# Optimization experiments

Measured on AMD Instinct MI355X. Metric: run time of the kernel, lower is better.

## Reference

```python
import jax, jax.numpy as jnp
import numpy as np

H = 768
F = 3072
NH = 12
EPS = 1e-5


def _layer_norm(x, g, b):
    mu = jnp.mean(x, axis=-1, keepdims=True)
    var = jnp.mean(jnp.square(x - mu), axis=-1, keepdims=True)
    return (x - mu) * jax.lax.rsqrt(var + EPS) * g + b


def setup_inputs() -> dict:
    key = jax.random.key(0)
    ks = jax.random.split(key, 16)
    s = 0.02
    d = {
        'x': jax.random.normal(ks[0], (2, 2048, H), jnp.float32),
        'Wq': jax.random.normal(ks[1], (H, H), jnp.float32) * s,
        'bq': jnp.zeros((H,), jnp.float32),
        'Wk': jax.random.normal(ks[2], (H, H), jnp.float32) * s,
        'bk': jnp.zeros((H,), jnp.float32),
        'Wv': jax.random.normal(ks[3], (H, H), jnp.float32) * s,
        'bv': jnp.zeros((H,), jnp.float32),
        'Wa1': jax.random.normal(ks[4], (H, H), jnp.float32) * s,
        'ba1': jnp.zeros((H,), jnp.float32),
        'g1': jnp.ones((H,), jnp.float32),
        'be1': jnp.zeros((H,), jnp.float32),
        'W1': jax.random.normal(ks[5], (H, F), jnp.float32) * s,
        'b1': jnp.zeros((F,), jnp.float32),
        'W2': jax.random.normal(ks[6], (F, H), jnp.float32) * s,
        'b2': jnp.zeros((H,), jnp.float32),
        'Wa2': jax.random.normal(ks[7], (H, H), jnp.float32) * s,
        'ba2': jnp.zeros((H,), jnp.float32),
        'g2': jnp.ones((H,), jnp.float32),
        'be2': jnp.zeros((H,), jnp.float32),
    }
    return d


def reference(x, Wq, bq, Wk, bk, Wv, bv, Wa1, ba1, g1, be1, W1, b1, W2, b2, Wa2, ba2, g2, be2):
    B, S, _ = x.shape
    Dh = H // NH
    # multi-head attention (naive: explicit scores + softmax)
    q = (x @ Wq + bq).reshape(B, S, NH, Dh)
    k = (x @ Wk + bk).reshape(B, S, NH, Dh)
    v = (x @ Wv + bv).reshape(B, S, NH, Dh)
    scores = jnp.einsum('bqhd,bkhd->bhqk', q, k) / jnp.sqrt(jnp.float32(Dh))
    att = jax.nn.softmax(scores, axis=-1)
    ctx = jnp.einsum('bhqk,bkhd->bqhd', att, v).reshape(B, S, H)
    # add_norm_1: Linear -> LayerNorm, then residual added AFTER LN (as in source)
    an1 = _layer_norm(ctx @ Wa1 + ba1, g1, be1) + x
    # feed-forward with exact GELU (torch nn.GELU default)
    ff = jax.nn.gelu(an1 @ W1 + b1, approximate=False) @ W2 + b2
    # add_norm_2: Linear -> LayerNorm, residual after LN
    out = _layer_norm(ff @ Wa2 + ba2, g2, be2) + an1
    return out
```

## Files before the change

kernel.cpp:

```cpp
#include <hip/hip_runtime.h>
#include <stdint.h>
#include <stddef.h>

#define HD 768
#define FF 3072
#define NHEAD 12
#define DHEAD 64
#define SEQ 2048
#define BATCH 2
#define NTOK (SEQ*BATCH)
#define SM_SCALE 0.18033688f

typedef __attribute__((ext_vector_type(8))) __bf16 bf16x8;
typedef __attribute__((ext_vector_type(4))) float f32x4;

__device__ __forceinline__ unsigned short f2bf(float f) {
  unsigned int u = __builtin_bit_cast(unsigned int, f);
  u += 0x7fffu + ((u >> 16) & 1u);
  return (unsigned short)(u >> 16);
}
__device__ __forceinline__ float bf2f(unsigned int s) {
  unsigned int u = s << 16;
  return __builtin_bit_cast(float, u);
}
__device__ __forceinline__ float4 ld4bf(const unsigned short* p) {
  uint2 w = *reinterpret_cast<const uint2*>(p);
  float4 o;
  o.x = bf2f(w.x & 0xffffu); o.y = bf2f(w.x >> 16);
  o.z = bf2f(w.y & 0xffffu); o.w = bf2f(w.y >> 16);
  return o;
}

__device__ __forceinline__ void gl16(const unsigned short* g, unsigned short* l) {
  __builtin_amdgcn_global_load_lds(
      (const __attribute__((address_space(1))) void*)g,
      (__attribute__((address_space(3))) void*)l,
      16, 0, 0);
}

__global__ void k_prep(const float* __restrict__ Wq, const float* __restrict__ Wk,
                       const float* __restrict__ Wv, const float* __restrict__ Wa1,
                       const float* __restrict__ W1, const float* __restrict__ W2,
                       const float* __restrict__ Wa2,
                       unsigned short* __restrict__ WqkvT, unsigned short* __restrict__ Wa1T,
                       unsigned short* __restrict__ W1T, unsigned short* __restrict__ W2T,
                       unsigned short* __restrict__ Wa2T,
                       const float* __restrict__ x, unsigned short* __restrict__ xb, int n4,
                       const float* __restrict__ bq, const float* __restrict__ bk,
                       const float* __restrict__ bv, float* __restrict__ biasqkv) {
  int t = blockIdx.x;
  int tid = threadIdx.x;
  if (t >= 7488) {
    int tb = t - 7488;
    if (tb < 9) {
      int idx = tb * 256 + tid;
      if (idx < 3*HD) {
        float v = idx < HD ? bq[idx] : idx < 2*HD ? bk[idx-HD] : bv[idx-2*HD];
        biasqkv[idx] = v;
      }
    }
    int i = tb * 256 + tid;
    int stride = 2048 * 256;
    for (; i < n4; i += stride) {
      float4 v = reinterpret_cast<const float4*>(x)[i];
      ushort4 o;
      o.x = f2bf(v.x); o.y = f2bf(v.y); o.z = f2bf(v.z); o.w = f2bf(v.w);
      reinterpret_cast<ushort4*>(xb)[i] = o;
    }
    return;
  }
  __shared__ float tile[32][33];
  const float* in; unsigned short* out; int K, N;
  if (t < 2304)      { int seg = t / 576; t -= seg * 576; K = HD; N = HD;
                       in  = seg==0 ? Wq : seg==1 ? Wk : seg==2 ? Wv : Wa1;
                       out = seg<3 ? WqkvT + seg*HD*HD : Wa1T; }
  else if (t < 4608) { t -= 2304; in = W1;  out = W1T;  K = HD; N = FF; }
  else if (t < 6912) { t -= 4608; in = W2;  out = W2T;  K = FF; N = HD; }
  else               { t -= 6912; in = Wa2; out = Wa2T; K = HD; N = HD; }
  int nt = N / 32;
  int nb = (t % nt) * 32, kb = (t / nt) * 32;
  int tx = tid & 31, ty = tid >> 5;
  for (int i = ty; i < 32; i += 8)
    tile[i][tx] = in[(size_t)(kb + i) * N + nb + tx];
  __syncthreads();
  for (int i = ty; i < 32; i += 8)
    out[(size_t)(nb + i) * K + kb + tx] = f2bf(tile[tx][i]);
}

__global__ void k_vtrans(const unsigned short* __restrict__ qkv, unsigned short* __restrict__ vt) {
  __shared__ unsigned short tile[32][33];
  int st = blockIdx.x * 32;
  int ct = blockIdx.y * 32;
  int b = blockIdx.z;
  int tx = threadIdx.x, ty = threadIdx.y;
  for (int i = ty; i < 32; i += 8)
    tile[i][tx] = qkv[(size_t)(b*SEQ + st + i) * 2304 + 2*HD + ct + tx];
  __syncthreads();
  for (int i = ty; i < 32; i += 8) {
    int vcol = ct + i;
    int p = st + tx;
    int k64 = p & 63;
    int news = (p & ~63) + ((k64 >> 2) & 3) * 16 + (k64 >> 4) * 4 + (k64 & 3);
    vt[((size_t)(b*NHEAD + (vcol >> 6)) * DHEAD + (vcol & 63)) * SEQ + news] = tile[tx][i];
  }
}


#define BN 128
#define BK 64

template<int MODE, int TBM>
__global__ __launch_bounds__(256, 3)
void k_gemm(const unsigned short* __restrict__ A, const unsigned short* __restrict__ Bt,
            const float* __restrict__ bias, void* __restrict__ Cout,
            int M, int N, int K) {
  constexpr int MR = TBM / 32;
  constexpr int AI = TBM / 32;
  __shared__ unsigned short As[TBM*BK];
  __shared__ unsigned short Bs[BN*BK];
  int tid = threadIdx.x;
  int bm = blockIdx.x * TBM;
  int bn = blockIdx.y * BN;
  int wave = tid >> 6, lane = tid & 63;
  int wm = wave >> 1, wn = wave & 1;
  int wr = wm * (TBM/2);
  int wc = wn * 64;
  int fr = lane & 15;
  int hi = lane >> 4;

  f32x4 acc[MR][4];
#pragma unroll
  for (int m = 0; m < MR; ++m)
#pragma unroll
    for (int n = 0; n < 4; ++n) acc[m][n] = (f32x4){0.f,0.f,0.f,0.f};

  int g8 = lane >> 3;
  int cc = (lane & 7) ^ g8;
  int arow = (TBM/4)*wave + g8;
  int brow = 32*wave + g8;
  const unsigned short* ag = A + (size_t)(bm + arow) * K + cc*8;
  const unsigned short* bg = Bt + (size_t)(bn + brow) * K + cc*8;
  unsigned short* asl = As + (TBM/4)*wave*BK;
  unsigned short* bsl = Bs + 32*wave*BK;

  for (int k0 = 0; k0 < K; k0 += BK) {
#pragma unroll
    for (int i = 0; i < AI; ++i)
      gl16(ag + (size_t)(8*i)*K + k0, asl + (8*i)*BK);
#pragma unroll
    for (int i = 0; i < 4; ++i)
      gl16(bg + (size_t)(8*i)*K + k0, bsl + (8*i)*BK);
    __syncthreads();

    bf16x8 af[MR][2], bf[4][2];
#pragma unroll
    for (int m = 0; m < MR; ++m) {
      int R = wr + m*16 + fr, sw = R & 7;
#pragma unroll
      for (int h2 = 0; h2 < 2; ++h2)
        af[m][h2] = __builtin_bit_cast(bf16x8,
          *reinterpret_cast<const uint4*>(&As[R*BK + ((hi + h2*4) ^ sw)*8]));
    }
#pragma unroll
    for (int n = 0; n < 4; ++n) {
      int R = wc + n*16 + fr, sw = R & 7;
#pragma unroll
      for (int h2 = 0; h2 < 2; ++h2)
        bf[n][h2] = __builtin_bit_cast(bf16x8,
          *reinterpret_cast<const uint4*>(&Bs[R*BK + ((hi + h2*4) ^ sw)*8]));
    }
#pragma unroll
    for (int m = 0; m < MR; ++m)
#pragma unroll
      for (int n = 0; n < 4; ++n) {
        acc[m][n] = __builtin_amdgcn_mfma_f32_16x16x32_bf16(af[m][0], bf[n][0], acc[m][n], 0, 0, 0);
        acc[m][n] = __builtin_amdgcn_mfma_f32_16x16x32_bf16(af[m][1], bf[n][1], acc[m][n], 0, 0, 0);
      }
    __syncthreads();
  }

  int crow0 = (lane >> 4) * 4;
  int ccol = lane & 15;
#pragma unroll
  for (int m = 0; m < MR; ++m) {
#pragma unroll
    for (int n = 0; n < 4; ++n) {
      int gcol = bn + wc + n*16 + ccol;
      float bv_ = bias[gcol];
#pragma unroll
      for (int r = 0; r < 4; ++r) {
        int grow = bm + wr + m*16 + crow0 + r;
        float v = acc[m][n][r] + bv_;
        if (MODE == 2) v = 0.5f * v * (1.0f + erff(v * 0.70710678118f));
        if (MODE == 3 && gcol < HD) v *= SM_SCALE;
        reinterpret_cast<unsigned short*>(Cout)[(size_t)grow * N + gcol] = f2bf(v);
      }
    }
  }
}


#define KVB 64
#define KP 72

__global__ __launch_bounds__(256, 3)
void k_attn_mfma(const unsigned short* __restrict__ qkv,
                 const unsigned short* __restrict__ vt,
                 unsigned short* __restrict__ ctx) {
  __shared__ unsigned short Ks[KVB][KP];
  __shared__ unsigned short Vt[DHEAD][KP];
  __shared__ f32x4 Mg[2][9][64];

  int tid = threadIdx.x;
  int wv = tid >> 6, lane = tid & 63;
  int lo = lane & 15, hi = lane >> 4;
  int qh = wv & 1;
  int kh = wv >> 1;

  int lin = blockIdx.x + 32*(blockIdx.y + NHEAD*blockIdx.z);
  int nl = (lin & 7) * 96 + (lin >> 3);
  int qb = nl & 31;
  int rest = nl >> 5;
  int h = rest % NHEAD;
  int b = rest / NHEAD;
  int q0 = qb * 64;

  const unsigned short* qpA = qkv + (size_t)(b*SEQ + q0 + qh*32 + lo) * 2304 + h*DHEAD + hi*8;
  const unsigned short* qpB = qpA + (size_t)16 * 2304;
  bf16x8 qfA0 = __builtin_bit_cast(bf16x8, *reinterpret_cast<const uint4*>(qpA));
  bf16x8 qfA1 = __builtin_bit_cast(bf16x8, *reinterpret_cast<const uint4*>(qpA + 32));
  bf16x8 qfB0 = __builtin_bit_cast(bf16x8, *reinterpret_cast<const uint4*>(qpB));
  bf16x8 qfB1 = __builtin_bit_cast(bf16x8, *reinterpret_cast<const uint4*>(qpB + 32));

  f32x4 poA[4], poB[4];
#pragma unroll
  for (int dt = 0; dt < 4; ++dt) { poA[dt] = (f32x4){0.f,0.f,0.f,0.f}; poB[dt] = (f32x4){0.f,0.f,0.f,0.f}; }
  float lrA = 0.f, lrB = 0.f;

  int sr = tid >> 2, scg = (tid & 3) * 16;
  const unsigned short* kgl = qkv + (size_t)(b*SEQ)*2304 + HD + h*DHEAD;
  const unsigned short* vgl = vt + ((size_t)(b*NHEAD + h)) * DHEAD * SEQ;

  for (int t0 = 0; t0 < SEQ; t0 += KVB) {
    const unsigned short* kp = kgl + (size_t)(t0 + sr)*2304 + scg;
    const unsigned short* vp = vgl + (size_t)sr*SEQ + t0 + scg;
    uint4 ku0 = *reinterpret_cast<const uint4*>(kp);
    uint4 ku1 = *reinterpret_cast<const uint4*>(kp + 8);
    uint4 vu0 = *reinterpret_cast<const uint4*>(vp);
    uint4 vu1 = *reinterpret_cast<const uint4*>(vp + 8);
    __syncthreads();
    *reinterpret_cast<uint4*>(&Ks[sr][scg])     = ku0;
    *reinterpret_cast<uint4*>(&Ks[sr][scg + 8]) = ku1;
    *reinterpret_cast<uint4*>(&Vt[sr][scg])     = vu0;
    *reinterpret_cast<uint4*>(&Vt[sr][scg + 8]) = vu1;
    __syncthreads();

    f32x4 sA[2], sB[2];
#pragma unroll
    for (int kg = 0; kg < 2; ++kg) {
      int krow = kh*32 + kg*16 + lo;
      bf16x8 a0 = __builtin_bit_cast(bf16x8, *reinterpret_cast<const uint4*>(&Ks[krow][hi*8]));
      bf16x8 a1 = __builtin_bit_cast(bf16x8, *reinterpret_cast<const uint4*>(&Ks[krow][32 + hi*8]));
      f32x4 s = (f32x4){0.f,0.f,0.f,0.f};
      s = __builtin_amdgcn_mfma_f32_16x16x32_bf16(a0, qfA0, s, 0, 0, 0);
      s = __builtin_amdgcn_mfma_f32_16x16x32_bf16(a1, qfA1, s, 0, 0, 0);
      sA[kg] = s;
      s = (f32x4){0.f,0.f,0.f,0.f};
      s = __builtin_amdgcn_mfma_f32_16x16x32_bf16(a0, qfB0, s, 0, 0, 0);
      s = __builtin_amdgcn_mfma_f32_16x16x32_bf16(a1, qfB1, s, 0, 0, 0);
      sB[kg] = s;
    }

    unsigned int pwA[4], pwB[4];
#pragma unroll
    for (int kg = 0; kg < 2; ++kg) {
      float a0 = exp2f(sA[kg][0]), a1 = exp2f(sA[kg][1]);
      float a2 = exp2f(sA[kg][2]), a3 = exp2f(sA[kg][3]);
      lrA += a0 + a1 + a2 + a3;
      asm("v_cvt_pk_bf16_f32 %0, %1, %2" : "=v"(pwA[kg*2])   : "v"(a0), "v"(a1));
      asm("v_cvt_pk_bf16_f32 %0, %1, %2" : "=v"(pwA[kg*2+1]) : "v"(a2), "v"(a3));
      float b0 = exp2f(sB[kg][0]), b1 = exp2f(sB[kg][1]);
      float b2 = exp2f(sB[kg][2]), b3 = exp2f(sB[kg][3]);
      lrB += b0 + b1 + b2 + b3;
      asm("v_cvt_pk_bf16_f32 %0, %1, %2" : "=v"(pwB[kg*2])   : "v"(b0), "v"(b1));
      asm("v_cvt_pk_bf16_f32 %0, %1, %2" : "=v"(pwB[kg*2+1]) : "v"(b2), "v"(b3));
    }

    uint4 uA; uA.x = pwA[0]; uA.y = pwA[1]; uA.z = pwA[2]; uA.w = pwA[3];
    uint4 uB; uB.x = pwB[0]; uB.y = pwB[1]; uB.z = pwB[2]; uB.w = pwB[3];
    bf16x8 paA = __builtin_bit_cast(bf16x8, uA);
    bf16x8 paB = __builtin_bit_cast(bf16x8, uB);

#pragma unroll
    for (int dt = 0; dt < 4; ++dt) {
      int col = dt*16 + lo;
      bf16x8 vv = __builtin_bit_cast(bf16x8, *reinterpret_cast<const uint4*>(&Vt[col][hi*16 + kh*8]));
      poA[dt] = __builtin_amdgcn_mfma_f32_16x16x32_bf16(paA, vv, poA[dt], 0, 0, 0);
      poB[dt] = __builtin_amdgcn_mfma_f32_16x16x32_bf16(paB, vv, poB[dt], 0, 0, 0);
    }
  }

  if (kh == 1) {
#pragma unroll
    for (int dt = 0; dt < 4; ++dt) {
      Mg[qh][dt][lane] = poA[dt];
      Mg[qh][4 + dt][lane] = poB[dt];
    }
    Mg[qh][8][lane] = (f32x4){lrA, lrB, 0.f, 0.f};
  }
  __syncthreads();
  if (kh == 0) {
#pragma unroll
    for (int dt = 0; dt < 4; ++dt) {
      f32x4 mA = Mg[qh][dt][lane], mB = Mg[qh][4 + dt][lane];
      poA[dt][0] += mA[0]; poA[dt][1] += mA[1]; poA[dt][2] += mA[2]; poA[dt][3] += mA[3];
      poB[dt][0] += mB[0]; poB[dt][1] += mB[1]; poB[dt][2] += mB[2]; poB[dt][3] += mB[3];
    }
    f32x4 lm = Mg[qh][8][lane];
    lrA += lm[0]; lrB += lm[1];
    lrA += __shfl_xor(lrA, 16); lrA += __shfl_xor(lrA, 32);
    lrB += __shfl_xor(lrB, 16); lrB += __shfl_xor(lrB, 32);

    unsigned short* op = ctx + (size_t)(b*SEQ + q0 + qh*32) * HD + h*DHEAD;
#pragma unroll
    for (int r = 0; r < 4; ++r) {
      float LA = __shfl(lrA, hi*4 + r);
      float LB = __shfl(lrB, hi*4 + r);
      float liA = (LA > 0.f) ? 1.0f / LA : 0.f;
      float liB = (LB > 0.f) ? 1.0f / LB : 0.f;
      int row = hi*4 + r;
#pragma unroll
      for (int dt = 0; dt < 4; ++dt) {
        op[(size_t)row*HD + dt*16 + lo]        = f2bf(poA[dt][r] * liA);
        op[(size_t)(16 + row)*HD + dt*16 + lo] = f2bf(poB[dt][r] * liB);
      }
    }
  }
}

template<int RESID_BF16, int WRITE_F32>
__global__ __launch_bounds__(256, 4)
void k_ln(const unsigned short* __restrict__ xin, const void* __restrict__ resid_,
          const float* __restrict__ g, const float* __restrict__ be,
          float* __restrict__ outf, unsigned short* __restrict__ outb) {
  int wave = threadIdx.x >> 6, lane = threadIdx.x & 63;
  int row = blockIdx.x * 4 + wave;
  const unsigned short* xp = xin + (size_t)row * HD;
  const float4* gp = reinterpret_cast<const float4*>(g);
  const float4* bp = reinterpret_cast<const float4*>(be);
  float4 v[3];
  float sum = 0.f, sq = 0.f;
#pragma unroll
  for (int i = 0; i < 3; ++i) {
    v[i] = ld4bf(xp + (lane + 64*i)*4);
    sum += v[i].x + v[i].y + v[i].z + v[i].w;
    sq  += v[i].x*v[i].x + v[i].y*v[i].y + v[i].z*v[i].z + v[i].w*v[i].w;
  }
#pragma unroll
  for (int m = 1; m < 64; m <<= 1) { sum += __shfl_xor(sum, m); sq += __shfl_xor(sq, m); }
  float mean = sum * (1.0f/768.0f);
  float var = sq * (1.0f/768.0f) - mean*mean;
  float rstd = rsqrtf(var + 1e-5f);
#pragma unroll
  for (int i = 0; i < 3; ++i) {
    float4 gg = gp[lane + 64*i], bb = bp[lane + 64*i];
    float4 rr;
    if (RESID_BF16)
      rr = ld4bf((const unsigned short*)resid_ + (size_t)row * HD + (lane + 64*i)*4);
    else
      rr = reinterpret_cast<const float4*>((const float*)resid_ + (size_t)row * HD)[lane + 64*i];
    float4 o;
    o.x = (v[i].x - mean)*rstd*gg.x + bb.x + rr.x;
    o.y = (v[i].y - mean)*rstd*gg.y + bb.y + rr.y;
    o.z = (v[i].z - mean)*rstd*gg.z + bb.z + rr.z;
    o.w = (v[i].w - mean)*rstd*gg.w + bb.w + rr.w;
    if (WRITE_F32) {
      reinterpret_cast<float4*>(outf + (size_t)row * HD)[lane + 64*i] = o;
    } else {
      ushort4 ob;
      ob.x = f2bf(o.x); ob.y = f2bf(o.y); ob.z = f2bf(o.z); ob.w = f2bf(o.w);
      reinterpret_cast<ushort4*>(outb + (size_t)row * HD)[lane + 64*i] = ob;
    }
  }
}


extern "C" void kernel_launch(void* const* d_in, const int* in_sizes, int n_in,
                              void* d_out, int out_size, void* d_ws, size_t ws_size,
                              hipStream_t stream) {
  const float* x   = (const float*)d_in[0];
  const float* Wq  = (const float*)d_in[1];
  const float* bq  = (const float*)d_in[2];
  const float* Wk  = (const float*)d_in[3];
  const float* bk  = (const float*)d_in[4];
  const float* Wv  = (const float*)d_in[5];
  const float* bv  = (const float*)d_in[6];
  const float* Wa1 = (const float*)d_in[7];
  const float* ba1 = (const float*)d_in[8];
  const float* g1  = (const float*)d_in[9];
  const float* be1 = (const float*)d_in[10];
  const float* W1  = (const float*)d_in[11];
  const float* b1  = (const float*)d_in[12];
  const float* W2  = (const float*)d_in[13];
  const float* b2  = (const float*)d_in[14];
  const float* Wa2 = (const float*)d_in[15];
  const float* ba2 = (const float*)d_in[16];
  const float* g2  = (const float*)d_in[17];
  const float* be2 = (const float*)d_in[18];

  char* ws = (char*)d_ws;
  size_t off = 0;
  auto alloc = [&](size_t bytes) -> void* {
    void* p = ws + off;
    off += (bytes + 255) & ~(size_t)255;
    return p;
  };
  unsigned short* xb    = (unsigned short*)alloc((size_t)NTOK*HD*2);
  unsigned short* WqkvT = (unsigned short*)alloc((size_t)3*HD*HD*2);
  unsigned short* Wa1T  = (unsigned short*)alloc((size_t)HD*HD*2);
  unsigned short* W1T   = (unsigned short*)alloc((size_t)FF*HD*2);
  unsigned short* W2T   = (unsigned short*)alloc((size_t)HD*FF*2);
  unsigned short* Wa2T  = (unsigned short*)alloc((size_t)HD*HD*2);
  float*          biasqkv = (float*)alloc((size_t)3*HD*4);
  unsigned short* qkvb  = (unsigned short*)alloc((size_t)NTOK*3*HD*2);
  unsigned short* vtb   = (unsigned short*)alloc((size_t)NTOK*HD*2);
  unsigned short* ctxb  = (unsigned short*)alloc((size_t)NTOK*HD*2);
  unsigned short* a1b   = (unsigned short*)alloc((size_t)NTOK*HD*2);
  unsigned short* an1b  = (unsigned short*)alloc((size_t)NTOK*HD*2);
  unsigned short* h1g   = (unsigned short*)alloc((size_t)NTOK*FF*2);
  unsigned short* f2b   = (unsigned short*)alloc((size_t)NTOK*HD*2);
  unsigned short* a2b   = (unsigned short*)alloc((size_t)NTOK*HD*2);
  (void)ws_size; (void)in_sizes; (void)n_in; (void)out_size;

  dim3 t32x8(32, 8);
  k_prep<<<9536, 256, 0, stream>>>(Wq, Wk, Wv, Wa1, W1, W2, Wa2,
                                   WqkvT, Wa1T, W1T, W2T, Wa2T,
                                   x, xb, NTOK*HD/4, bq, bk, bv, biasqkv);

  k_gemm<3,128><<<dim3(NTOK/128, 2304/BN), 256, 0, stream>>>(xb, WqkvT, biasqkv, qkvb, NTOK, 3*HD, HD);
  k_vtrans<<<dim3(SEQ/32, HD/32, BATCH), t32x8, 0, stream>>>(qkvb, vtb);
  k_attn_mfma<<<dim3(SEQ/64, NHEAD, BATCH), 256, 0, stream>>>(qkvb, vtb, ctxb);
  k_gemm<1,64><<<dim3(NTOK/64, HD/BN), 256, 0, stream>>>(ctxb, Wa1T, ba1, a1b, NTOK, HD, HD);
  k_ln<0,0><<<NTOK/4, 256, 0, stream>>>(a1b, x, g1, be1, nullptr, an1b);
  k_gemm<2,128><<<dim3(NTOK/128, FF/BN), 256, 0, stream>>>(an1b, W1T, b1, h1g, NTOK, FF, HD);
  k_gemm<1,64><<<dim3(NTOK/64, HD/BN), 256, 0, stream>>>(h1g, W2T, b2, f2b, NTOK, HD, FF);
  k_gemm<1,64><<<dim3(NTOK/64, HD/BN), 256, 0, stream>>>(f2b, Wa2T, ba2, a2b, NTOK, HD, HD);
  k_ln<1,1><<<NTOK/4, 256, 0, stream>>>(a2b, an1b, g2, be2, (float*)d_out, nullptr);
}
```

Baseline: 192.1 us.

## Fuse V transpose into QKV GEMM epilogue, remap GEMM blocks, use tanh GELU

```diff
diff --git a/kernel.cpp b/kernel.cpp
--- a/kernel.cpp
+++ b/kernel.cpp
@@ -87,24 +87,6 @@
     out[(size_t)(nb + i) * K + kb + tx] = f2bf(tile[tx][i]);
 }
 
-__global__ void k_vtrans(const unsigned short* __restrict__ qkv, unsigned short* __restrict__ vt) {
-  __shared__ unsigned short tile[32][33];
-  int st = blockIdx.x * 32;
-  int ct = blockIdx.y * 32;
-  int b = blockIdx.z;
-  int tx = threadIdx.x, ty = threadIdx.y;
-  for (int i = ty; i < 32; i += 8)
-    tile[i][tx] = qkv[(size_t)(b*SEQ + st + i) * 2304 + 2*HD + ct + tx];
-  __syncthreads();
-  for (int i = ty; i < 32; i += 8) {
-    int vcol = ct + i;
-    int p = st + tx;
-    int k64 = p & 63;
-    int news = (p & ~63) + ((k64 >> 2) & 3) * 16 + (k64 >> 4) * 4 + (k64 & 3);
-    vt[((size_t)(b*NHEAD + (vcol >> 6)) * DHEAD + (vcol & 63)) * SEQ + news] = tile[tx][i];
-  }
-}
-
 
 #define BN 128
 #define BK 64
@@ -113,14 +95,18 @@
 __global__ __launch_bounds__(256, 3)
 void k_gemm(const unsigned short* __restrict__ A, const unsigned short* __restrict__ Bt,
             const float* __restrict__ bias, void* __restrict__ Cout,
+            unsigned short* __restrict__ Vout,
             int M, int N, int K) {
   constexpr int MR = TBM / 32;
   constexpr int AI = TBM / 32;
   __shared__ unsigned short As[TBM*BK];
   __shared__ unsigned short Bs[BN*BK];
   int tid = threadIdx.x;
-  int bm = blockIdx.x * TBM;
-  int bn = blockIdx.y * BN;
+  int nwg = gridDim.x * gridDim.y;
+  int lin = blockIdx.x + gridDim.x * blockIdx.y;
+  int nl = (lin & 7) * (nwg >> 3) + (lin >> 3);
+  int bm = (nl % gridDim.x) * TBM;
+  int bn = (nl / gridDim.x) * BN;
   int wave = tid >> 6, lane = tid & 63;
   int wm = wave >> 1, wn = wave & 1;
   int wr = wm * (TBM/2);
@@ -181,6 +167,37 @@
 
   int crow0 = (lane >> 4) * 4;
   int ccol = lane & 15;
+
+  if (MODE == 3 && bn >= 2*HD) {
+    unsigned short* tb = (wave < 2) ? As + wave*4096 : Bs + (wave-2)*4096;
+#pragma unroll
+    for (int m = 0; m < MR; ++m)
+#pragma unroll
+      for (int n = 0; n < 4; ++n)
+#pragma unroll
+        for (int r = 0; r < 4; ++r) {
+          int tl = m*16 + crow0 + r;
+          int cl = n*16 + ccol;
+          float v = acc[m][n][r] + bias[bn + wc + cl];
+          int pt = ((tl>>2)&3)*16 + ((tl>>4)<<2) + (tl&3);
+          tb[cl*64 + (((pt>>3) ^ (cl&7))<<3) + (pt&7)] = f2bf(v);
+        }
+    __syncthreads();
+    int tk0 = bm + wr;
+    int bb = tk0 >> 11;
+    int sb = tk0 & 2047;
+    int hh = (bn + wc - 2*HD) >> 6;
+    unsigned short* dst = Vout + ((size_t)(bb*NHEAD + hh) * DHEAD) * SEQ + sb;
+#pragma unroll
+    for (int p = 0; p < 8; ++p) {
+      int dr = p*8 + (lane >> 3);
+      int cj = lane & 7;
+      uint4 w = *reinterpret_cast<const uint4*>(&tb[dr*64 + ((cj ^ (dr&7))<<3)]);
+      *reinterpret_cast<uint4*>(dst + (size_t)dr*SEQ + cj*8) = w;
+    }
+    return;
+  }
+
 #pragma unroll
   for (int m = 0; m < MR; ++m) {
 #pragma unroll
@@ -191,7 +208,10 @@
       for (int r = 0; r < 4; ++r) {
         int grow = bm + wr + m*16 + crow0 + r;
         float v = acc[m][n][r] + bv_;
-        if (MODE == 2) v = 0.5f * v * (1.0f + erff(v * 0.70710678118f));
+        if (MODE == 2) {
+          float a = v + 0.044715f * v * v * v;
+          v = v / (1.0f + exp2f(-2.3022082f * a));
+        }
         if (MODE == 3 && gcol < HD) v *= SM_SCALE;
         reinterpret_cast<unsigned short*>(Cout)[(size_t)grow * N + gcol] = f2bf(v);
       }
@@ -432,18 +452,16 @@
   unsigned short* a2b   = (unsigned short*)alloc((size_t)NTOK*HD*2);
   (void)ws_size; (void)in_sizes; (void)n_in; (void)out_size;
 
-  dim3 t32x8(32, 8);
   k_prep<<<9536, 256, 0, stream>>>(Wq, Wk, Wv, Wa1, W1, W2, Wa2,
                                    WqkvT, Wa1T, W1T, W2T, Wa2T,
                                    x, xb, NTOK*HD/4, bq, bk, bv, biasqkv);
 
-  k_gemm<3,128><<<dim3(NTOK/128, 2304/BN), 256, 0, stream>>>(xb, WqkvT, biasqkv, qkvb, NTOK, 3*HD, HD);
-  k_vtrans<<<dim3(SEQ/32, HD/32, BATCH), t32x8, 0, stream>>>(qkvb, vtb);
+  k_gemm<3,128><<<dim3(NTOK/128, 2304/BN), 256, 0, stream>>>(xb, WqkvT, biasqkv, qkvb, vtb, NTOK, 3*HD, HD);
   k_attn_mfma<<<dim3(SEQ/64, NHEAD, BATCH), 256, 0, stream>>>(qkvb, vtb, ctxb);
-  k_gemm<1,64><<<dim3(NTOK/64, HD/BN), 256, 0, stream>>>(ctxb, Wa1T, ba1, a1b, NTOK, HD, HD);
+  k_gemm<1,64><<<dim3(NTOK/64, HD/BN), 256, 0, stream>>>(ctxb, Wa1T, ba1, a1b, nullptr, NTOK, HD, HD);
   k_ln<0,0><<<NTOK/4, 256, 0, stream>>>(a1b, x, g1, be1, nullptr, an1b);
-  k_gemm<2,128><<<dim3(NTOK/128, FF/BN), 256, 0, stream>>>(an1b, W1T, b1, h1g, NTOK, FF, HD);
-  k_gemm<1,64><<<dim3(NTOK/64, HD/BN), 256, 0, stream>>>(h1g, W2T, b2, f2b, NTOK, HD, FF);
-  k_gemm<1,64><<<dim3(NTOK/64, HD/BN), 256, 0, stream>>>(f2b, Wa2T, ba2, a2b, NTOK, HD, HD);
+  k_gemm<2,128><<<dim3(NTOK/128, FF/BN), 256, 0, stream>>>(an1b, W1T, b1, h1g, nullptr, NTOK, FF, HD);
+  k_gemm<1,64><<<dim3(NTOK/64, HD/BN), 256, 0, stream>>>(h1g, W2T, b2, f2b, nullptr, NTOK, HD, FF);
+  k_gemm<1,64><<<dim3(NTOK/64, HD/BN), 256, 0, stream>>>(f2b, Wa2T, ba2, a2b, nullptr, NTOK, HD, HD);
   k_ln<1,1><<<NTOK/4, 256, 0, stream>>>(a2b, an1b, g2, be2, (float*)d_out, nullptr);
 }
```

Result: no change. 192.4 us (+0.2%).
